# Performance work log

Hardware: AMD Instinct MI355X
Metric: run time of the kernel (lower is better)

Reference implementation:

```python
import jax, jax.numpy as jnp
import numpy as np
from jax import lax

B, T, F = 128, 100, 64
HID = [16, 32]  # encoder hidden dims; decoder uses reversed [32, 16]
K = 3


def _conv2d(x, w, b):
    # x: [N, Cin, H, W], w: [Cout, Cin, kh, kw] -> 'SAME' padding as in torch padding=k//2
    y = lax.conv_general_dilated(x, w, (1, 1), 'SAME',
                                 dimension_numbers=('NCHW', 'OIHW', 'NCHW'))
    return y + b[None, :, None, None]


def _convlstm_layer(xs, w, b, h0, c0):
    # xs: [T, B, Cin, H, W] time-major; returns hidden seq [T,B,Chid,H,W] and final (h, c)
    def step(carry, x_t):
        h, c = carry
        z = _conv2d(jnp.concatenate([x_t, h], axis=1), w, b)
        i, f, o, g = jnp.split(z, 4, axis=1)  # gate order i, f, o, g
        c2 = jax.nn.sigmoid(f) * c + jax.nn.sigmoid(i) * jnp.tanh(g)
        h2 = jax.nn.sigmoid(o) * jnp.tanh(c2)
        return (h2, c2), h2
    (hT, cT), hs = lax.scan(step, (h0, c0), xs)
    return hs, (hT, cT)


def setup_inputs() -> dict:
    key = jax.random.key(0)
    ks = jax.random.split(key, 12)
    s = 0.05
    inp = {
        'x': jax.random.normal(ks[0], (B, T, F), dtype=jnp.float32),
        # encoder layer 0: in=1+16, out=4*16
        'enc_w0': jax.random.normal(ks[1], (4 * HID[0], 1 + HID[0], K, K), dtype=jnp.float32) * s,
        'enc_b0': jnp.zeros((4 * HID[0],), dtype=jnp.float32),
        # encoder layer 1: in=16+32, out=4*32
        'enc_w1': jax.random.normal(ks[2], (4 * HID[1], HID[0] + HID[1], K, K), dtype=jnp.float32) * s,
        'enc_b1': jnp.zeros((4 * HID[1],), dtype=jnp.float32),
        # decoder layer 0: hidden=32, input=32 (last encoder hidden)
        'dec_w0': jax.random.normal(ks[3], (4 * HID[1], HID[1] + HID[1], K, K), dtype=jnp.float32) * s,
        'dec_b0': jnp.zeros((4 * HID[1],), dtype=jnp.float32),
        # decoder layer 1: hidden=16, input=32
        'dec_w1': jax.random.normal(ks[4], (4 * HID[0], HID[1] + HID[0], K, K), dtype=jnp.float32) * s,
        'dec_b1': jnp.zeros((4 * HID[0],), dtype=jnp.float32),
        # final 1x1 conv: 16 -> 1
        'fc_w': jax.random.normal(ks[5], (1, HID[0], 1, 1), dtype=jnp.float32) * s,
        'fc_b': jnp.zeros((1,), dtype=jnp.float32),
    }
    return inp


def reference(x, enc_w0, enc_b0, enc_w1, enc_b1, dec_w0, dec_b0, dec_w1, dec_b1, fc_w, fc_b):
    b, t, f = x.shape
    # [b,t,f] -> [t,b,1,f,1] time-major, spatial (f,1)
    xs = jnp.transpose(x.reshape(b, t, 1, f, 1), (1, 0, 2, 3, 4))
    z16 = jnp.zeros((b, HID[0], f, 1), x.dtype)
    z32 = jnp.zeros((b, HID[1], f, 1), x.dtype)

    enc1, (h1, c1) = _convlstm_layer(xs, enc_w0, enc_b0, z16, z16)
    enc2, (h2, c2) = _convlstm_layer(enc1, enc_w1, enc_b1, z32, z32)

    # decoder initial states = encoder final states reversed
    dec1, _ = _convlstm_layer(enc2, dec_w0, dec_b0, h2, c2)
    dec2, _ = _convlstm_layer(dec1, dec_w1, dec_b1, h1, c1)  # [t,b,16,f,1]

    # final 1x1 conv applied per timestep == one batched conv over t*b
    flat = dec2.reshape(t * b, HID[0], f, 1)
    out = _conv2d(flat, fc_w, fc_b)  # [t*b,1,f,1]
    recon = jnp.transpose(out.reshape(t, b, f), (1, 0, 2))  # [b,t,f]
    return recon
```

## Files before the change

kernel.cpp:

```cpp
#include <hip/hip_runtime.h>
#include <math.h>

#define B_ 128
#define T_ 100
#define RS 72
#define RS2 40

__device__ __forceinline__ float frcp_(float x){ return __builtin_amdgcn_rcpf(x); }
__device__ __forceinline__ float fsig_(float x){ return frcp_(1.f + __expf(-x)); }
__device__ __forceinline__ float ftanh_(float x){ float e = __expf(2.f*x); return 1.f - 2.f*frcp_(e+1.f); }
__device__ __forceinline__ float gate1(float zi, float zf, float zo, float zg, float& c){
    float cc = fsig_(zf)*c + fsig_(zi)*ftanh_(zg);
    c = cc;
    return fsig_(zo)*ftanh_(cc);
}
__device__ __forceinline__ float4 ldf4(const float* p){ return *reinterpret_cast<const float4*>(p); }
__device__ __forceinline__ void stf4(float* p, float4 v){ *reinterpret_cast<float4*>(p) = v; }
__device__ __forceinline__ float2 ldf2(const float* p){ return *reinterpret_cast<const float2*>(p); }
__device__ __forceinline__ void stf2(float* p, float2 v){ *reinterpret_cast<float2*>(p) = v; }
__device__ __forceinline__ float4 add4(float4 a, float4 b){
    return make_float4(a.x+b.x, a.y+b.y, a.z+b.z, a.w+b.w);
}
__device__ __forceinline__ float4 gate4(float4 zi, float4 zf, float4 zo, float4 zg,
                                        float bi, float bf, float bo, float bg, float4& c){
    float4 h;
    h.x = gate1(zi.x+bi, zf.x+bf, zo.x+bo, zg.x+bg, c.x);
    h.y = gate1(zi.y+bi, zf.y+bf, zo.y+bo, zg.y+bg, c.y);
    h.z = gate1(zi.z+bi, zf.z+bf, zo.z+bo, zg.z+bg, c.z);
    h.w = gate1(zi.w+bi, zf.w+bf, zo.w+bo, zg.w+bg, c.w);
    return h;
}

__device__ __forceinline__ void fma4v(float w, float u0,float u1,float u2,float u3, float4& a){
    a.x = fmaf(w,u0,a.x); a.y = fmaf(w,u1,a.y);
    a.z = fmaf(w,u2,a.z); a.w = fmaf(w,u3,a.w);
}
__device__ __forceinline__ void fma2v(float w, float u0,float u1, float2& a){
    a.x = fmaf(w,u0,a.x); a.y = fmaf(w,u1,a.y);
}

template<int ROWS>
__device__ __forceinline__ void rowacc4(const float* __restrict__ rowp,
                                        const float* __restrict__ wk,
                                        float4& ai, float4& af, float4& ao, float4& ag)
{
    float  m = rowp[-1];
    float4 a = ldf4(rowp);
    float  p = rowp[4];
    float4 wa = ldf4(wk);
    float4 wb = ldf4(wk + ROWS);
    float4 wc = ldf4(wk + 2*ROWS);
    fma4v(wa.x, m,a.x,a.y,a.z, ai);  fma4v(wa.y, m,a.x,a.y,a.z, af);
    fma4v(wa.z, m,a.x,a.y,a.z, ao);  fma4v(wa.w, m,a.x,a.y,a.z, ag);
    fma4v(wb.x, a.x,a.y,a.z,a.w, ai); fma4v(wb.y, a.x,a.y,a.z,a.w, af);
    fma4v(wb.z, a.x,a.y,a.z,a.w, ao); fma4v(wb.w, a.x,a.y,a.z,a.w, ag);
    fma4v(wc.x, a.y,a.z,a.w,p, ai);  fma4v(wc.y, a.y,a.z,a.w,p, af);
    fma4v(wc.z, a.y,a.z,a.w,p, ao);  fma4v(wc.w, a.y,a.z,a.w,p, ag);
}
template<int ROWS>
__device__ __forceinline__ void rowacc2(const float* __restrict__ rowp,
                                        const float* __restrict__ wk,
                                        float2& ai, float2& af, float2& ao, float2& ag)
{
    float  m = rowp[-1];
    float2 a = *reinterpret_cast<const float2*>(rowp);
    float  p = rowp[2];
    float4 wa = ldf4(wk);
    float4 wb = ldf4(wk + ROWS);
    float4 wc = ldf4(wk + 2*ROWS);
    fma2v(wa.x, m,a.x, ai); fma2v(wa.y, m,a.x, af);
    fma2v(wa.z, m,a.x, ao); fma2v(wa.w, m,a.x, ag);
    fma2v(wb.x, a.x,a.y, ai); fma2v(wb.y, a.x,a.y, af);
    fma2v(wb.z, a.x,a.y, ao); fma2v(wb.w, a.x,a.y, ag);
    fma2v(wc.x, a.y,p, ai); fma2v(wc.y, a.y,p, af);
    fma2v(wc.z, a.y,p, ao); fma2v(wc.w, a.y,p, ag);
}
template<int ROWS>
__device__ __forceinline__ void rowacc8(const float* __restrict__ rowp,
                                        const float* __restrict__ wk,
                                        float4& i0, float4& i1, float4& f0v, float4& f1v,
                                        float4& o0, float4& o1, float4& g0, float4& g1)
{
    float  m = rowp[-1];
    float4 a = ldf4(rowp);
    float4 b = ldf4(rowp + 4);
    float  p = rowp[8];
    float4 wa = ldf4(wk);
    float4 wb = ldf4(wk + ROWS);
    float4 wc = ldf4(wk + 2*ROWS);
    fma4v(wa.x, m,a.x,a.y,a.z, i0);   fma4v(wa.x, a.w,b.x,b.y,b.z, i1);
    fma4v(wa.y, m,a.x,a.y,a.z, f0v);  fma4v(wa.y, a.w,b.x,b.y,b.z, f1v);
    fma4v(wa.z, m,a.x,a.y,a.z, o0);   fma4v(wa.z, a.w,b.x,b.y,b.z, o1);
    fma4v(wa.w, m,a.x,a.y,a.z, g0);   fma4v(wa.w, a.w,b.x,b.y,b.z, g1);
    fma4v(wb.x, a.x,a.y,a.z,a.w, i0); fma4v(wb.x, b.x,b.y,b.z,b.w, i1);
    fma4v(wb.y, a.x,a.y,a.z,a.w, f0v);fma4v(wb.y, b.x,b.y,b.z,b.w, f1v);
    fma4v(wb.z, a.x,a.y,a.z,a.w, o0); fma4v(wb.z, b.x,b.y,b.z,b.w, o1);
    fma4v(wb.w, a.x,a.y,a.z,a.w, g0); fma4v(wb.w, b.x,b.y,b.z,b.w, g1);
    fma4v(wc.x, a.y,a.z,a.w,b.x, i0); fma4v(wc.x, b.y,b.z,b.w,p, i1);
    fma4v(wc.y, a.y,a.z,a.w,b.x, f0v);fma4v(wc.y, b.y,b.z,b.w,p, f1v);
    fma4v(wc.z, a.y,a.z,a.w,b.x, o0); fma4v(wc.z, b.y,b.z,b.w,p, o1);
    fma4v(wc.w, a.y,a.z,a.w,b.x, g0); fma4v(wc.w, b.y,b.z,b.w,p, g1);
}

__global__ __launch_bounds__(1024, 4) void enc_kernel(
    const float* __restrict__ x,
    const float* __restrict__ w0, const float* __restrict__ b0,
    const float* __restrict__ w1, const float* __restrict__ b1,
    float* __restrict__ seq,
    float* __restrict__ h1f, float* __restrict__ c1f,
    float* __restrict__ h2f, float* __restrict__ c2f,
    float* __restrict__ comm, int* __restrict__ flags)
{
    __shared__ float wl0[51 * 64];
    __shared__ float wl1[144 * 128];
    __shared__ float bs0[64];
    __shared__ float bs1[128];
    __shared__ float hbuf[50 * RS2];
    __shared__ float zsA[2048];
    __shared__ float zsB3[3 * 4096];

    const int tid = threadIdx.x;
    const int b = blockIdx.x & 127;
    const int s = blockIdx.x >> 7;
    const int gofs = s << 5;
    const int g  = tid >> 8;
    const int r  = tid & 255;
    const int chB = r >> 3, f0B = (r & 7) * 4;
    const int chA = r >> 4, f0A = (r & 15) * 2;
    const int haloSlot = s ? 3 : 36;
    const int myId = (b << 1) | s;
    const int peerId = myId ^ 1;
    float* mySend = &comm[(size_t)myId * 128];
    const float* peerBuf = &comm[(size_t)peerId * 128];

    for (int idx = tid; idx < 51 * 64; idx += 1024) {
        int k = idx >> 6, rr = idx & 63;
        int ch = rr >> 2, gg = rr & 3;
        int ci = k / 3, d = k - ci * 3;
        wl0[idx] = w0[((gg * 16 + ch) * 17 + ci) * 9 + d * 3 + 1];
    }
    for (int idx = tid; idx < 144 * 128; idx += 1024) {
        int k = idx >> 7, rr = idx & 127;
        int ch = rr >> 2, gg = rr & 3;
        int ci = k / 3, d = k - ci * 3;
        wl1[idx] = w1[((gg * 32 + ch) * 48 + ci) * 9 + d * 3 + 1];
    }
    if (tid < 64) bs0[tid] = b0[tid];
    if (tid < 128) bs1[tid] = b1[tid];
    for (int i = tid; i < 50 * RS2; i += 1024) hbuf[i] = 0.f;
    __syncthreads();

    const int xl = tid - 256;
    if (xl >= 0 && xl < 34) {
        const int gc = gofs - 1 + xl;
        const bool v = (gc >= 0) && (gc < 64);
        hbuf[0 * RS2 + 3 + xl] = v ? x[(b * T_ + 0) * 64 + gc] : 0.f;
        hbuf[1 * RS2 + 3 + xl] = v ? x[(b * T_ + 1) * 64 + gc] : 0.f;
    }
    const float biA = bs0[chA], bfA = bs0[16+chA], boA = bs0[32+chA], bgA = bs0[48+chA];
    const float biB = bs1[chB], bfB = bs1[32+chB], boB = bs1[64+chB], bgB = bs1[96+chB];
    __syncthreads();

    const float4 z4 = make_float4(0.f, 0.f, 0.f, 0.f);
    const float2 z2 = make_float2(0.f, 0.f);
    float2 c0q = z2;
    float4 c1a = z4;

    if (g == 2) {
        float2 ai = z2, af = z2, ao = z2, ag = z2;
        rowacc2<64>(&hbuf[0 * RS2 + 4 + f0A], &wl0[chA * 4], ai, af, ao, ag);
        float2 hq;
        hq.x = gate1(ai.x + biA, af.x + bfA, ao.x + boA, ag.x + bgA, c0q.x);
        hq.y = gate1(ai.y + biA, af.y + bfA, ao.y + boA, ag.y + bgA, c0q.y);
        *reinterpret_cast<float2*>(&hbuf[(2 + chA) * RS2 + 4 + f0A]) = hq;
        if ((r & 15) == (s ? 0 : 15)) {
            const float v = s ? hq.x : hq.y;
            __hip_atomic_store((unsigned int*)&mySend[1 * 64 + 32 + chA],
                               __float_as_uint(v),
                               __ATOMIC_RELAXED, __HIP_MEMORY_SCOPE_AGENT);
        }
    }
    __syncthreads();

#pragma unroll 1
    for (int t = 0; t < T_; ++t) {
        if (tid == 0)
            __hip_atomic_store(&flags[myId], t + 1,
                               __ATOMIC_RELAXED, __HIP_MEMORY_SCOPE_AGENT);
        if (tid < 48 && (t > 0 || tid >= 32)) {
            while (__hip_atomic_load(&flags[peerId],
                                     __ATOMIC_ACQUIRE, __HIP_MEMORY_SCOPE_AGENT) < t + 1)
                __builtin_amdgcn_s_sleep(2);
            const int par = (t + 1) & 1;
            const unsigned int uv =
                __hip_atomic_load((const unsigned int*)&peerBuf[par * 64 + tid],
                                  __ATOMIC_RELAXED, __HIP_MEMORY_SCOPE_AGENT);
            const float v = __uint_as_float(uv);
            if (tid < 32) hbuf[(18 + tid) * RS2 + haloSlot] = v;
            else          hbuf[(2 + (tid - 32)) * RS2 + haloSlot] = v;
        }
        __syncthreads();

        const bool doL0 = (t + 1 < T_);
        float4 I = z4, F = z4, O = z4, G = z4;
#pragma unroll 1
        for (int j = 0; j < 12; ++j) {
            const int ci = 12 * g + j;
            rowacc4<128>(&hbuf[(2 + ci) * RS2 + 4 + f0B],
                         &wl1[(ci * 3) * 128 + chB * 4], I, F, O, G);
        }
        float2 ai = z2, af = z2, ao = z2, ag = z2;
        if (doL0) {
            if (g == 2) {
                rowacc2<64>(&hbuf[((t + 1) & 1) * RS2 + 4 + f0A], &wl0[chA * 4],
                            ai, af, ao, ag);
#pragma unroll 1
                for (int j = 0; j < 8; ++j)
                    rowacc2<64>(&hbuf[(2 + j) * RS2 + 4 + f0A],
                                &wl0[((1 + j) * 3) * 64 + chA * 4], ai, af, ao, ag);
            } else if (g == 3) {
#pragma unroll 1
                for (int j = 8; j < 16; ++j)
                    rowacc2<64>(&hbuf[(2 + j) * RS2 + 4 + f0A],
                                &wl0[((1 + j) * 3) * 64 + chA * 4], ai, af, ao, ag);
            }
        }
        if (g != 0) {
            float* zp = &zsB3[(g - 1) * 4096 + r * 4];
            stf4(zp, I); stf4(zp + 1024, F); stf4(zp + 2048, O); stf4(zp + 3072, G);
        }
        if (g == 3 && doL0) {
            float* zp = &zsA[r * 2];
            stf2(zp, ai); stf2(zp + 512, af); stf2(zp + 1024, ao); stf2(zp + 1536, ag);
        }
        if (xl >= 0 && xl < 34 && t + 2 < T_) {
            const int gc = gofs - 1 + xl;
            hbuf[(t & 1) * RS2 + 3 + xl] =
                (gc >= 0 && gc < 64) ? x[(b * T_ + t + 2) * 64 + gc] : 0.f;
        }
        __syncthreads();
        if (g == 0) {
            const float* p0 = &zsB3[0 * 4096 + r * 4];
            const float* p1 = &zsB3[1 * 4096 + r * 4];
            const float* p2 = &zsB3[2 * 4096 + r * 4];
            float4 zi = add4(add4(I, ldf4(p0)),        add4(ldf4(p1),        ldf4(p2)));
            float4 zf = add4(add4(F, ldf4(p0 + 1024)), add4(ldf4(p1 + 1024), ldf4(p2 + 1024)));
            float4 zo = add4(add4(O, ldf4(p0 + 2048)), add4(ldf4(p1 + 2048), ldf4(p2 + 2048)));
            float4 zg = add4(add4(G, ldf4(p0 + 3072)), add4(ldf4(p1 + 3072), ldf4(p2 + 3072)));
            float4 hq = gate4(zi, zf, zo, zg, biB, bfB, boB, bgB, c1a);
            stf4(&hbuf[(18 + chB) * RS2 + 4 + f0B], hq);
            stf4(&seq[((size_t)t * B_ + b) * 2048 + chB * 64 + gofs + f0B], hq);
            if (doL0 && (r & 7) == (s ? 0 : 7)) {
                const float v = s ? hq.x : hq.w;
                __hip_atomic_store((unsigned int*)&mySend[(t & 1) * 64 + chB],
                                   __float_as_uint(v),
                                   __ATOMIC_RELAXED, __HIP_MEMORY_SCOPE_AGENT);
            }
        }
        if (g == 2 && doL0) {
            float2 pzi = ldf2(&zsA[r * 2]);
            float2 pzf = ldf2(&zsA[512 + r * 2]);
            float2 pzo = ldf2(&zsA[1024 + r * 2]);
            float2 pzg = ldf2(&zsA[1536 + r * 2]);
            float2 hq2;
            hq2.x = gate1(ai.x+pzi.x+biA, af.x+pzf.x+bfA, ao.x+pzo.x+boA, ag.x+pzg.x+bgA, c0q.x);
            hq2.y = gate1(ai.y+pzi.y+biA, af.y+pzf.y+bfA, ao.y+pzo.y+boA, ag.y+pzg.y+bgA, c0q.y);
            *reinterpret_cast<float2*>(&hbuf[(2 + chA) * RS2 + 4 + f0A]) = hq2;
            if ((r & 15) == (s ? 0 : 15)) {
                const float v = s ? hq2.x : hq2.y;
                __hip_atomic_store((unsigned int*)&mySend[(t & 1) * 64 + 32 + chA],
                                   __float_as_uint(v),
                                   __ATOMIC_RELAXED, __HIP_MEMORY_SCOPE_AGENT);
            }
        }
        __syncthreads();
    }

    if (g == 2) {
        *reinterpret_cast<float2*>(&h1f[(b * 16 + chA) * 64 + gofs + f0A]) =
            *reinterpret_cast<const float2*>(&hbuf[(2 + chA) * RS2 + 4 + f0A]);
        *reinterpret_cast<float2*>(&c1f[(b * 16 + chA) * 64 + gofs + f0A]) = c0q;
    }
    if (g == 0) {
        stf4(&h2f[b * 2048 + chB * 64 + gofs + f0B],
             ldf4(&hbuf[(18 + chB) * RS2 + 4 + f0B]));
        stf4(&c2f[b * 2048 + chB * 64 + gofs + f0B], c1a);
    }
}

__global__ __launch_bounds__(256, 2) void xconv0_kernel(
    const float* __restrict__ seqIn, const float* __restrict__ w,
    float* __restrict__ zx, int t0)
{
    __shared__ float wl[96 * 128];
    __shared__ float xt[32 * RS];

    const int tid = threadIdx.x;
    const int tl = blockIdx.x / B_;
    const int b  = blockIdx.x - tl * B_;
    const int t  = t0 + tl;

    for (int idx = tid; idx < 96 * 128; idx += 256) {
        int k = idx >> 7, rr = idx & 127;
        int ch = rr >> 2, g = rr & 3;
        int ci = k / 3, d = k - ci * 3;
        wl[idx] = w[((g * 32 + ch) * 64 + ci) * 9 + d * 3 + 1];
    }
    {
        int rr = tid >> 3, j = tid & 7;
        xt[rr * RS + (j < 4 ? j : 64 + j)] = 0.f;
    }
    {
        const float* s = &seqIn[((size_t)t * B_ + b) * 2048 + tid * 8];
        float4 v0 = ldf4(s);
        float4 v1 = ldf4(s + 4);
        int ci = tid >> 3, col = (tid & 7) * 8;
        stf4(&xt[ci * RS + 4 + col], v0);
        stf4(&xt[ci * RS + 4 + col + 4], v1);
    }
    __syncthreads();

    const int ch = tid >> 3, f0 = (tid & 7) * 8;
    const float4 z4 = make_float4(0.f,0.f,0.f,0.f);
    float4 i0=z4,i1=z4,f0v=z4,f1v=z4,o0=z4,o1=z4,g0=z4,g1=z4;
#pragma unroll 1
    for (int rr = 0; rr < 32; ++rr)
        rowacc8<128>(&xt[rr * RS + 4 + f0], wl + (rr * 3) * 128 + ch * 4,
                     i0, i1, f0v, f1v, o0, o1, g0, g1);

    float* zp = &zx[(((size_t)tl * B_ + b) * 4) * 2048 + ch * 64 + f0];
    stf4(zp, i0);            stf4(zp + 4, i1);
    stf4(zp + 2048, f0v);    stf4(zp + 2048 + 4, f1v);
    stf4(zp + 4096, o0);     stf4(zp + 4096 + 4, o1);
    stf4(zp + 6144, g0);     stf4(zp + 6144 + 4, g1);
}

__global__ __launch_bounds__(512, 1) void decg(
    const float* __restrict__ w0, const float* __restrict__ b0,
    const float* __restrict__ w1, const float* __restrict__ b1,
    const float* __restrict__ zx,
    const float* __restrict__ h0in, const float* __restrict__ c0in,
    const float* __restrict__ h1in, const float* __restrict__ c1in,
    float* __restrict__ h0sv, float* __restrict__ c0sv,
    float* __restrict__ h1sv, float* __restrict__ c1sv,
    const float* __restrict__ fw, const float* __restrict__ fb,
    float* __restrict__ out,
    float* __restrict__ comm0, float* __restrict__ comm1,
    int* __restrict__ flg, int t0, int tn, int lastc)
{
    __shared__ float wl0[96 * 128];
    __shared__ float wl1[144 * 64];
    __shared__ float hp0[32 * RS2];
    __shared__ float hp1[16 * RS2];
    __shared__ float zs0[4096];
    __shared__ float zs1[4 * 16 * 32];
    __shared__ float bs0[128];
    __shared__ float bs1[64];
    __shared__ float fcw[16];
    __shared__ float fcb_s;

    const int tid = threadIdx.x;
    const int b = blockIdx.x & 127;
    const int s = blockIdx.x >> 7;
    const int gofs = s << 5;
    const int haloSlot = s ? 3 : 36;
    const int bcol = s ? 31 : 32;
    const int myId = (b << 1) | s, peerId = myId ^ 1;
    float* send0 = &comm0[(size_t)myId * 64];
    const float* peer0 = &comm0[(size_t)peerId * 64];
    float* send1 = &comm1[(size_t)myId * 32];
    const float* peer1 = &comm1[(size_t)peerId * 32];

    const int kg = tid >> 8;
    const int r = tid & 255;
    const bool isD0 = (r < 128);
    const int ch0 = r >> 2, t0f = (r & 3) * 8;
    const int r1 = r - 128;
    const int ch1 = r1 >> 3, t1f = (r1 & 7) * 4;

    for (int idx = tid; idx < 96 * 128; idx += 512) {
        int k = idx >> 7, rr = idx & 127;
        int c8 = rr >> 2, g = rr & 3;
        int ci = k / 3, d = k - ci * 3;
        wl0[idx] = w0[((g * 32 + c8) * 64 + 32 + ci) * 9 + d * 3 + 1];
    }
    for (int idx = tid; idx < 144 * 64; idx += 512) {
        int k = idx >> 6, rr = idx & 63;
        int c8 = rr >> 2, g = rr & 3;
        int ci = k / 3, d = k - ci * 3;
        wl1[idx] = w1[((g * 16 + c8) * 48 + ci) * 9 + d * 3 + 1];
    }
    if (tid < 128) bs0[tid] = b0[tid];
    if (tid < 64) bs1[tid] = b1[tid];
    if (tid < 16) fcw[tid] = fw[tid];
    if (tid == 16) fcb_s = fb[0];
    for (int i = tid; i < 32 * RS2; i += 512) hp0[i] = 0.f;
    for (int i = tid; i < 16 * RS2; i += 512) hp1[i] = 0.f;
    __syncthreads();

    for (int i = tid; i < 1024; i += 512) {
        int c8 = i >> 5, f = i & 31;
        hp0[c8 * RS2 + 4 + f] = h0in[b * 2048 + c8 * 64 + gofs + f];
    }
    { int c8 = tid >> 5, f = tid & 31;
      hp1[c8 * RS2 + 4 + f] = h1in[b * 1024 + c8 * 64 + gofs + f]; }
    if (tid < 32) hp0[tid * RS2 + haloSlot] = h0in[b * 2048 + tid * 64 + bcol];
    if (tid >= 64 && tid < 80)
        hp1[(tid - 64) * RS2 + haloSlot] = h1in[b * 1024 + (tid - 64) * 64 + bcol];

    const float4 z4 = make_float4(0.f, 0.f, 0.f, 0.f);
    float4 c0a = z4, c0b = z4;
    float4 c1v = z4;
    float bi, bfv, bo, bg;
    if (isD0) { bi = bs0[ch0]; bfv = bs0[32+ch0]; bo = bs0[64+ch0]; bg = bs0[96+ch0]; }
    else      { bi = bs1[ch1]; bfv = bs1[16+ch1]; bo = bs1[32+ch1]; bg = bs1[48+ch1]; }
    if (kg == 0) {
        if (isD0) {
            c0a = ldf4(&c0in[b * 2048 + ch0 * 64 + gofs + t0f]);
            c0b = ldf4(&c0in[b * 2048 + ch0 * 64 + gofs + t0f + 4]);
        } else {
            c1v = ldf4(&c1in[b * 1024 + ch1 * 64 + gofs + t1f]);
        }
    }
    const float fcbv = fcb_s;

#pragma unroll 1
    for (int u = t0; u < t0 + tn + lastc; ++u) {
        if (tid == 0)
            __hip_atomic_store(&flg[myId], u,
                               __ATOMIC_RELAXED, __HIP_MEMORY_SCOPE_AGENT);
        if (u > t0) {
            const int par = (u - 1) & 1;
            if (tid < 32) {
                while (__hip_atomic_load(&flg[peerId],
                                         __ATOMIC_ACQUIRE, __HIP_MEMORY_SCOPE_AGENT) < u)
                    __builtin_amdgcn_s_sleep(2);
                hp0[tid * RS2 + haloSlot] = __uint_as_float(
                    __hip_atomic_load((const unsigned int*)&peer0[par * 32 + tid],
                                      __ATOMIC_RELAXED, __HIP_MEMORY_SCOPE_AGENT));
            } else if (tid >= 64 && tid < 80 && u >= 2) {
                while (__hip_atomic_load(&flg[peerId],
                                         __ATOMIC_ACQUIRE, __HIP_MEMORY_SCOPE_AGENT) < u)
                    __builtin_amdgcn_s_sleep(2);
                hp1[(tid - 64) * RS2 + haloSlot] = __uint_as_float(
                    __hip_atomic_load((const unsigned int*)&peer1[par * 16 + (tid - 64)],
                                      __ATOMIC_RELAXED, __HIP_MEMORY_SCOPE_AGENT));
            }
        }
        __syncthreads();

        const bool d0act = (u - t0 < tn);
        const bool d1act = (u >= 1);
        float4 A0=z4,A1=z4,B0=z4,B1=z4,C0=z4,C1=z4,D0=z4,D1=z4;
        float4 ai=z4, af=z4, ao=z4, ag=z4;
        float4 X0=z4,X1=z4,X2=z4,X3=z4,X4=z4,X5=z4,X6=z4,X7=z4;

        if (isD0) {
            if (d0act) {
                if (kg == 0) {
                    const float* zp = &zx[(((size_t)(u - t0) * B_ + b) * 4) * 2048
                                          + ch0 * 64 + gofs + t0f];
                    X0 = ldf4(zp);         X1 = ldf4(zp + 4);
                    X2 = ldf4(zp + 2048);  X3 = ldf4(zp + 2052);
                    X4 = ldf4(zp + 4096);  X5 = ldf4(zp + 4100);
                    X6 = ldf4(zp + 6144);  X7 = ldf4(zp + 6148);
                }
#pragma unroll 1
                for (int j = 0; j < 16; ++j) {
                    const int ci = kg * 16 + j;
                    rowacc8<128>(&hp0[ci * RS2 + 4 + t0f], &wl0[(ci * 3) * 128 + ch0 * 4],
                                 A0, A1, B0, B1, C0, C1, D0, D1);
                }
            }
            if (kg == 1 && r < 32 && u >= 2) {
                float a = fcbv;
#pragma unroll
                for (int k2 = 0; k2 < 16; ++k2)
                    a = fmaf(fcw[k2], hp1[k2 * RS2 + 4 + r], a);
                out[(b * T_ + (u - 2)) * 64 + gofs + r] = a;
            }
        } else if (d1act) {
            if (kg == 0) {
#pragma unroll 1
                for (int j = 0; j < 24; ++j)
                    rowacc4<64>(&hp0[j * RS2 + 4 + t1f], &wl1[(j * 3) * 64 + ch1 * 4],
                                ai, af, ao, ag);
            } else {
#pragma unroll 1
                for (int j = 24; j < 32; ++j)
                    rowacc4<64>(&hp0[j * RS2 + 4 + t1f], &wl1[(j * 3) * 64 + ch1 * 4],
                                ai, af, ao, ag);
#pragma unroll 1
                for (int j = 0; j < 16; ++j)
                    rowacc4<64>(&hp1[j * RS2 + 4 + t1f], &wl1[((32 + j) * 3) * 64 + ch1 * 4],
                                ai, af, ao, ag);
            }
        }
        if (kg == 1) {
            if (isD0) { if (d0act) {
                float* zp = &zs0[r * 4];
                stf4(zp + 0,    A0); stf4(zp + 512,  A1);
                stf4(zp + 1024, B0); stf4(zp + 1536, B1);
                stf4(zp + 2048, C0); stf4(zp + 2560, C1);
                stf4(zp + 3072, D0); stf4(zp + 3584, D1);
            }} else { if (d1act) {
                stf4(&zs1[(0*16+ch1)*32 + t1f], ai);
                stf4(&zs1[(1*16+ch1)*32 + t1f], af);
                stf4(&zs1[(2*16+ch1)*32 + t1f], ao);
                stf4(&zs1[(3*16+ch1)*32 + t1f], ag);
            }}
        }
        __syncthreads();
        if (kg == 0) {
            if (isD0 && d0act) {
                const float* zp = &zs0[r * 4];
                float4 zi0 = add4(add4(A0, X0), ldf4(zp));
                float4 zi1 = add4(add4(A1, X1), ldf4(zp + 512));
                float4 zf0 = add4(add4(B0, X2), ldf4(zp + 1024));
                float4 zf1 = add4(add4(B1, X3), ldf4(zp + 1536));
                float4 zo0 = add4(add4(C0, X4), ldf4(zp + 2048));
                float4 zo1 = add4(add4(C1, X5), ldf4(zp + 2560));
                float4 zg0 = add4(add4(D0, X6), ldf4(zp + 3072));
                float4 zg1 = add4(add4(D1, X7), ldf4(zp + 3584));
                float4 h0q0 = gate4(zi0, zf0, zo0, zg0, bi, bfv, bo, bg, c0a);
                float4 h0q1 = gate4(zi1, zf1, zo1, zg1, bi, bfv, bo, bg, c0b);
                stf4(&hp0[ch0 * RS2 + 4 + t0f], h0q0);
                stf4(&hp0[ch0 * RS2 + 4 + t0f + 4], h0q1);
                if ((r & 3) == (s ? 0 : 3)) {
                    __hip_atomic_store((unsigned int*)&send0[(u & 1) * 32 + ch0],
                                       __float_as_uint(s ? h0q0.x : h0q1.w),
                                       __ATOMIC_RELAXED, __HIP_MEMORY_SCOPE_AGENT);
                }
            } else if (!isD0 && d1act) {
                float4 zi = add4(ai, ldf4(&zs1[(0*16+ch1)*32 + t1f]));
                float4 zf = add4(af, ldf4(&zs1[(1*16+ch1)*32 + t1f]));
                float4 zo = add4(ao, ldf4(&zs1[(2*16+ch1)*32 + t1f]));
                float4 zg = add4(ag, ldf4(&zs1[(3*16+ch1)*32 + t1f]));
                float4 h1q = gate4(zi, zf, zo, zg, bi, bfv, bo, bg, c1v);
                stf4(&hp1[ch1 * RS2 + 4 + t1f], h1q);
                if ((r1 & 7) == (s ? 0 : 7)) {
                    __hip_atomic_store((unsigned int*)&send1[(u & 1) * 16 + ch1],
                                       __float_as_uint(s ? h1q.x : h1q.w),
                                       __ATOMIC_RELAXED, __HIP_MEMORY_SCOPE_AGENT);
                }
            }
        }
        __syncthreads();
    }

    if (lastc && tid < 32) {
        float a = fcbv;
#pragma unroll
        for (int k2 = 0; k2 < 16; ++k2)
            a = fmaf(fcw[k2], hp1[k2 * RS2 + 4 + tid], a);
        out[(b * T_ + (T_ - 1)) * 64 + gofs + tid] = a;
    }
    for (int i = tid; i < 1024; i += 512) {
        int c8 = i >> 5, f = i & 31;
        h0sv[b * 2048 + c8 * 64 + gofs + f] = hp0[c8 * RS2 + 4 + f];
    }
    { int c8 = tid >> 5, f = tid & 31;
      h1sv[b * 1024 + c8 * 64 + gofs + f] = hp1[c8 * RS2 + 4 + f]; }
    if (kg == 0) {
        if (isD0) {
            stf4(&c0sv[b * 2048 + ch0 * 64 + gofs + t0f], c0a);
            stf4(&c0sv[b * 2048 + ch0 * 64 + gofs + t0f + 4], c0b);
        } else {
            stf4(&c1sv[b * 1024 + ch1 * 64 + gofs + t1f], c1v);
        }
    }
}

__global__ __launch_bounds__(512, 1) void dec0_fb(
    const float* __restrict__ w, const float* __restrict__ bias,
    float* __restrict__ seq,
    const float* __restrict__ hin, const float* __restrict__ cin)
{
    __shared__ float wl[192 * 128];
    __shared__ float bs[128];
    __shared__ float xin[32 * RS];
    __shared__ float hp[32 * RS];

    const int tid = threadIdx.x;
    const int b = blockIdx.x;

    for (int idx = tid; idx < 192 * 128; idx += 512) {
        int k = idx >> 7, rr = idx & 127;
        int ch = rr >> 2, g = rr & 3;
        int ci = k / 3, d = k - ci * 3;
        wl[idx] = w[((g * 32 + ch) * 64 + ci) * 9 + d * 3 + 1];
    }
    if (tid < 128) bs[tid] = bias[tid];
    for (int i = tid; i < 32 * RS; i += 512) { xin[i] = 0.f; hp[i] = 0.f; }
    __syncthreads();
    {
        const float* hs = &hin[b * 2048 + tid * 4];
        float4 hv = ldf4(hs);
        int ci = tid >> 4, col = (tid & 15) * 4;
        stf4(&hp[ci * RS + 4 + col], hv);
    }
    const int ch = tid >> 4, f0 = (tid & 15) * 4;
    float4 cc = ldf4(&cin[b * 2048 + ch * 64 + f0]);
    const float bi = bs[ch], bf = bs[32 + ch], bo = bs[64 + ch], bg = bs[96 + ch];
    const float4 z4 = make_float4(0.f,0.f,0.f,0.f);

    float4 nx = ldf4(&seq[(size_t)b * 2048 + tid * 4]);

#pragma unroll 1
    for (int t = 0; t < T_; ++t) {
        {
            int ci = tid >> 4, col = (tid & 15) * 4;
            stf4(&xin[ci * RS + 4 + col], nx);
        }
        __syncthreads();
        if (t + 1 < T_)
            nx = ldf4(&seq[((size_t)(t + 1) * B_ + b) * 2048 + tid * 4]);
        float4 ai = z4, af = z4, ao = z4, ag = z4;
#pragma unroll 1
        for (int rr = 0; rr < 32; ++rr)
            rowacc4<128>(&xin[rr * RS + 4 + f0], wl + (rr * 3) * 128 + ch * 4, ai, af, ao, ag);
#pragma unroll 1
        for (int rr = 0; rr < 32; ++rr)
            rowacc4<128>(&hp[rr * RS + 4 + f0], wl + ((32 + rr) * 3) * 128 + ch * 4, ai, af, ao, ag);
        float4 hn = gate4(ai, af, ao, ag, bi, bf, bo, bg, cc);
        __syncthreads();
        stf4(&hp[ch * RS + 4 + f0], hn);
        stf4(&seq[((size_t)t * B_ + b) * 2048 + ch * 64 + f0], hn);
    }
}

__global__ __launch_bounds__(512, 1) void dec1_fb(
    const float* __restrict__ w, const float* __restrict__ bias,
    const float* __restrict__ seq,
    const float* __restrict__ hin, const float* __restrict__ cin,
    const float* __restrict__ fw, const float* __restrict__ fb,
    float* __restrict__ out)
{
    __shared__ float wl[144 * 64];
    __shared__ float bs[64];
    __shared__ float xin[32 * RS];
    __shared__ float hp[16 * RS];
    __shared__ float fcw[16];
    __shared__ float fcb;

    const int tid = threadIdx.x;
    const int b = blockIdx.x;

    for (int idx = tid; idx < 144 * 64; idx += 512) {
        int k = idx >> 6, rr = idx & 63;
        int ch = rr >> 2, g = rr & 3;
        int ci = k / 3, d = k - ci * 3;
        wl[idx] = w[((g * 16 + ch) * 48 + ci) * 9 + d * 3 + 1];
    }
    if (tid < 64) bs[tid] = bias[tid];
    if (tid < 16) fcw[tid] = fw[tid];
    if (tid == 16) fcb = fb[0];
    for (int i = tid; i < 32 * RS; i += 512) xin[i] = 0.f;
    for (int i = tid; i < 16 * RS; i += 512) hp[i] = 0.f;
    __syncthreads();
    {
        const float* hs = &hin[b * 1024 + tid * 2];
        float2 hv = *reinterpret_cast<const float2*>(hs);
        int ci = tid >> 5, col = (tid & 31) * 2;
        *reinterpret_cast<float2*>(&hp[ci * RS + 4 + col]) = hv;
    }
    const int ch = tid >> 5, f0 = (tid & 31) * 2;
    float2 cc = *reinterpret_cast<const float2*>(&cin[b * 1024 + ch * 64 + f0]);
    const float bi = bs[ch], bf = bs[16 + ch], bo = bs[32 + ch], bg = bs[48 + ch];
    const float2 z2 = make_float2(0.f,0.f);
    float4 nx = ldf4(&seq[(size_t)b * 2048 + tid * 4]);
    __syncthreads();

#pragma unroll 1
    for (int t = 0; t < T_; ++t) {
        {
            int ci = tid >> 4, col = (tid & 15) * 4;
            stf4(&xin[ci * RS + 4 + col], nx);
        }
        __syncthreads();
        if (t + 1 < T_)
            nx = ldf4(&seq[((size_t)(t + 1) * B_ + b) * 2048 + tid * 4]);

        float2 ai = z2, af = z2, ao = z2, ag = z2;
#pragma unroll 1
        for (int rr = 0; rr < 32; ++rr)
            rowacc2<64>(&xin[rr * RS + 4 + f0], wl + (rr * 3) * 64 + ch * 4, ai, af, ao, ag);
#pragma unroll 1
        for (int rr = 0; rr < 16; ++rr)
            rowacc2<64>(&hp[rr * RS + 4 + f0], wl + ((32 + rr) * 3) * 64 + ch * 4, ai, af, ao, ag);

        float2 hh;
        hh.x = gate1(ai.x + bi, af.x + bf, ao.x + bo, ag.x + bg, cc.x);
        hh.y = gate1(ai.y + bi, af.y + bf, ao.y + bo, ag.y + bg, cc.y);
        __syncthreads();
        *reinterpret_cast<float2*>(&hp[ch * RS + 4 + f0]) = hh;
        __syncthreads();

        if (tid < 64) {
            float a = fcb;
#pragma unroll
            for (int k2 = 0; k2 < 16; ++k2)
                a = fmaf(fcw[k2], hp[k2 * RS + 4 + tid], a);
            out[(b * T_ + t) * 64 + tid] = a;
        }
    }
}

extern "C" void kernel_launch(void* const* d_in, const int* in_sizes, int n_in,
                              void* d_out, int out_size, void* d_ws, size_t ws_size,
                              hipStream_t stream)
{
    (void)in_sizes; (void)n_in; (void)out_size;
    const float* x   = (const float*)d_in[0];
    const float* ew0 = (const float*)d_in[1];
    const float* eb0 = (const float*)d_in[2];
    const float* ew1 = (const float*)d_in[3];
    const float* eb1 = (const float*)d_in[4];
    const float* dw0 = (const float*)d_in[5];
    const float* db0 = (const float*)d_in[6];
    const float* dw1 = (const float*)d_in[7];
    const float* db1 = (const float*)d_in[8];
    const float* fw  = (const float*)d_in[9];
    const float* fb  = (const float*)d_in[10];
    float* out = (float*)d_out;

    float* ws  = (float*)d_ws;
    size_t off = 0;
    float* seq = ws + off; off += (size_t)T_ * B_ * 2048;
    float* h1f = ws + off; off += (size_t)B_ * 1024;
    float* c1f = ws + off; off += (size_t)B_ * 1024;
    float* h2f = ws + off; off += (size_t)B_ * 2048;
    float* c2f = ws + off; off += (size_t)B_ * 2048;
    float* hd0 = ws + off; off += (size_t)B_ * 2048;
    float* cd0 = ws + off; off += (size_t)B_ * 2048;
    float* hd1 = ws + off; off += (size_t)B_ * 1024;
    float* cd1 = ws + off; off += (size_t)B_ * 1024;
    float* comm = ws + off; off += 32768 + 16384 + 8192;
    int*   flg  = (int*)(ws + off); off += 1024;
    float* zx  = ws + off;

    float* commD0 = comm + 32768;
    float* commD1 = comm + 32768 + 16384;

    size_t availf = (ws_size / 4 > off) ? (ws_size / 4 - off) : 0;
    int TC = 0;
    if      (availf >= (size_t)100 * B_ * 8192) TC = 100;
    else if (availf >= (size_t)50  * B_ * 8192) TC = 50;
    else if (availf >= (size_t)25  * B_ * 8192) TC = 25;
    else if (availf >= (size_t)10  * B_ * 8192) TC = 10;

    hipMemsetAsync(flg, 0, 512 * sizeof(int), stream);
    enc_kernel<<<256, 1024, 0, stream>>>(x, ew0, eb0, ew1, eb1, seq,
                                         h1f, c1f, h2f, c2f, comm, flg);

    if (TC > 0) {
        for (int t0 = 0; t0 < T_; t0 += TC) {
            int tn = (t0 + TC <= T_) ? TC : (T_ - t0);
            int lastc = (t0 + tn >= T_) ? 1 : 0;
            xconv0_kernel<<<tn * B_, 256, 0, stream>>>(seq, dw0, zx, t0);
            decg<<<256, 512, 0, stream>>>(
                dw0, db0, dw1, db1, zx,
                t0 == 0 ? h2f : hd0, t0 == 0 ? c2f : cd0,
                t0 == 0 ? h1f : hd1, t0 == 0 ? c1f : cd1,
                hd0, cd0, hd1, cd1,
                fw, fb, out, commD0, commD1, flg + 256, t0, tn, lastc);
        }
    } else {
        dec0_fb<<<B_, 512, 0, stream>>>(dw0, db0, seq, h2f, c2f);
        dec1_fb<<<B_, 512, 0, stream>>>(dw1, db1, seq, h1f, c1f, fw, fb, out);
    }
}
```

Measured before the change: 2.008 ms.

## Double decoder block threads and split recurrent conv reductions across more groups

The fused decoder kernel now runs with 1024 threads per block instead of 512. Decoder layer 0 gives each thread 4 output columns instead of 8. Decoder layer 1 splits its 48 input rows across four 12-row groups and sums the partials through a larger shared-memory buffer. The goal is to shorten the per-timestep critical path of this latency-bound serial recurrence by spreading each step over more threads. In exchange it adds more partial-sum shared-memory traffic. The launch bound of (1024, 4) may also force a tight register budget and cause spills.

New measurement: 1.940 ms. -3.4%, faster.

```diff
diff --git a/kernel.cpp b/kernel.cpp
--- a/kernel.cpp
+++ b/kernel.cpp
@@ -335,7 +335,7 @@
     stf4(zp + 6144, g0);     stf4(zp + 6144 + 4, g1);
 }
 
-__global__ __launch_bounds__(512, 1) void decg(
+__global__ __launch_bounds__(1024, 4) void decg(
     const float* __restrict__ w0, const float* __restrict__ b0,
     const float* __restrict__ w1, const float* __restrict__ b1,
     const float* __restrict__ zx,
@@ -353,7 +353,7 @@
     __shared__ float hp0[32 * RS2];
     __shared__ float hp1[16 * RS2];
     __shared__ float zs0[4096];
-    __shared__ float zs1[4 * 16 * 32];
+    __shared__ float zs1_3[3 * 2048];
     __shared__ float bs0[128];
     __shared__ float bs1[64];
     __shared__ float fcw[16];
@@ -371,20 +371,22 @@
     float* send1 = &comm1[(size_t)myId * 32];
     const float* peer1 = &comm1[(size_t)peerId * 32];
 
-    const int kg = tid >> 8;
-    const int r = tid & 255;
-    const bool isD0 = (r < 128);
-    const int ch0 = r >> 2, t0f = (r & 3) * 8;
-    const int r1 = r - 128;
-    const int ch1 = r1 >> 3, t1f = (r1 & 7) * 4;
-
-    for (int idx = tid; idx < 96 * 128; idx += 512) {
+    const bool isD0 = (tid < 512);
+    const int sub = tid & 511;
+    const int kg = sub >> 8;
+    const int r = sub & 255;
+    const int ch0 = r >> 3, t0f = (r & 7) * 4;
+    const int d1g = sub >> 7;
+    const int rg1 = sub & 127;
+    const int ch1 = rg1 >> 3, t1f = (rg1 & 7) * 4;
+
+    for (int idx = tid; idx < 96 * 128; idx += 1024) {
         int k = idx >> 7, rr = idx & 127;
         int c8 = rr >> 2, g = rr & 3;
         int ci = k / 3, d = k - ci * 3;
         wl0[idx] = w0[((g * 32 + c8) * 64 + 32 + ci) * 9 + d * 3 + 1];
     }
-    for (int idx = tid; idx < 144 * 64; idx += 512) {
+    for (int idx = tid; idx < 144 * 64; idx += 1024) {
         int k = idx >> 6, rr = idx & 63;
         int c8 = rr >> 2, g = rr & 3;
         int ci = k / 3, d = k - ci * 3;
@@ -394,34 +396,31 @@
     if (tid < 64) bs1[tid] = b1[tid];
     if (tid < 16) fcw[tid] = fw[tid];
     if (tid == 16) fcb_s = fb[0];
-    for (int i = tid; i < 32 * RS2; i += 512) hp0[i] = 0.f;
-    for (int i = tid; i < 16 * RS2; i += 512) hp1[i] = 0.f;
+    for (int i = tid; i < 32 * RS2; i += 1024) hp0[i] = 0.f;
+    for (int i = tid; i < 16 * RS2; i += 1024) hp1[i] = 0.f;
     __syncthreads();
 
-    for (int i = tid; i < 1024; i += 512) {
-        int c8 = i >> 5, f = i & 31;
+    {
+        int c8 = tid >> 5, f = tid & 31;
         hp0[c8 * RS2 + 4 + f] = h0in[b * 2048 + c8 * 64 + gofs + f];
-    }
-    { int c8 = tid >> 5, f = tid & 31;
-      hp1[c8 * RS2 + 4 + f] = h1in[b * 1024 + c8 * 64 + gofs + f]; }
+        if (tid < 512)
+            hp1[(tid >> 5) * RS2 + 4 + (tid & 31)] =
+                h1in[b * 1024 + (tid >> 5) * 64 + gofs + (tid & 31)];
+    }
     if (tid < 32) hp0[tid * RS2 + haloSlot] = h0in[b * 2048 + tid * 64 + bcol];
     if (tid >= 64 && tid < 80)
         hp1[(tid - 64) * RS2 + haloSlot] = h1in[b * 1024 + (tid - 64) * 64 + bcol];
 
     const float4 z4 = make_float4(0.f, 0.f, 0.f, 0.f);
-    float4 c0a = z4, c0b = z4;
+    float4 c0v = z4;
     float4 c1v = z4;
     float bi, bfv, bo, bg;
     if (isD0) { bi = bs0[ch0]; bfv = bs0[32+ch0]; bo = bs0[64+ch0]; bg = bs0[96+ch0]; }
     else      { bi = bs1[ch1]; bfv = bs1[16+ch1]; bo = bs1[32+ch1]; bg = bs1[48+ch1]; }
-    if (kg == 0) {
-        if (isD0) {
-            c0a = ldf4(&c0in[b * 2048 + ch0 * 64 + gofs + t0f]);
-            c0b = ldf4(&c0in[b * 2048 + ch0 * 64 + gofs + t0f + 4]);
-        } else {
-            c1v = ldf4(&c1in[b * 1024 + ch1 * 64 + gofs + t1f]);
-        }
-    }
+    if (isD0 && kg == 0)
+        c0v = ldf4(&c0in[b * 2048 + ch0 * 64 + gofs + t0f]);
+    if (!isD0 && d1g == 0)
+        c1v = ldf4(&c1in[b * 1024 + ch1 * 64 + gofs + t1f]);
     const float fcbv = fcb_s;
 
 #pragma unroll 1
@@ -451,25 +450,24 @@
 
         const bool d0act = (u - t0 < tn);
         const bool d1act = (u >= 1);
-        float4 A0=z4,A1=z4,B0=z4,B1=z4,C0=z4,C1=z4,D0=z4,D1=z4;
-        float4 ai=z4, af=z4, ao=z4, ag=z4;
-        float4 X0=z4,X1=z4,X2=z4,X3=z4,X4=z4,X5=z4,X6=z4,X7=z4;
+        float4 ai = z4, af = z4, ao = z4, ag = z4;
+        float4 xi = z4, xf = z4, xo = z4, xg = z4;
 
         if (isD0) {
             if (d0act) {
                 if (kg == 0) {
                     const float* zp = &zx[(((size_t)(u - t0) * B_ + b) * 4) * 2048
                                           + ch0 * 64 + gofs + t0f];
-                    X0 = ldf4(zp);         X1 = ldf4(zp + 4);
-                    X2 = ldf4(zp + 2048);  X3 = ldf4(zp + 2052);
-                    X4 = ldf4(zp + 4096);  X5 = ldf4(zp + 4100);
-                    X6 = ldf4(zp + 6144);  X7 = ldf4(zp + 6148);
+                    xi = ldf4(zp);
+                    xf = ldf4(zp + 2048);
+                    xo = ldf4(zp + 4096);
+                    xg = ldf4(zp + 6144);
                 }
 #pragma unroll 1
                 for (int j = 0; j < 16; ++j) {
                     const int ci = kg * 16 + j;
-                    rowacc8<128>(&hp0[ci * RS2 + 4 + t0f], &wl0[(ci * 3) * 128 + ch0 * 4],
-                                 A0, A1, B0, B1, C0, C1, D0, D1);
+                    rowacc4<128>(&hp0[ci * RS2 + 4 + t0f], &wl0[(ci * 3) * 128 + ch0 * 4],
+                                 ai, af, ao, ag);
                 }
             }
             if (kg == 1 && r < 32 && u >= 2) {
@@ -480,69 +478,57 @@
                 out[(b * T_ + (u - 2)) * 64 + gofs + r] = a;
             }
         } else if (d1act) {
-            if (kg == 0) {
-#pragma unroll 1
-                for (int j = 0; j < 24; ++j)
-                    rowacc4<64>(&hp0[j * RS2 + 4 + t1f], &wl1[(j * 3) * 64 + ch1 * 4],
-                                ai, af, ao, ag);
-            } else {
-#pragma unroll 1
-                for (int j = 24; j < 32; ++j)
-                    rowacc4<64>(&hp0[j * RS2 + 4 + t1f], &wl1[(j * 3) * 64 + ch1 * 4],
-                                ai, af, ao, ag);
-#pragma unroll 1
-                for (int j = 0; j < 16; ++j)
-                    rowacc4<64>(&hp1[j * RS2 + 4 + t1f], &wl1[((32 + j) * 3) * 64 + ch1 * 4],
-                                ai, af, ao, ag);
-            }
-        }
-        if (kg == 1) {
-            if (isD0) { if (d0act) {
+            const int rlo = 12 * d1g, rhi = rlo + 12;
+            const int xhi = rhi < 32 ? rhi : 32;
+            const int hlo = rlo > 32 ? rlo : 32;
+#pragma unroll 1
+            for (int rr = rlo; rr < xhi; ++rr)
+                rowacc4<64>(&hp0[rr * RS2 + 4 + t1f], &wl1[(rr * 3) * 64 + ch1 * 4],
+                            ai, af, ao, ag);
+#pragma unroll 1
+            for (int rr = hlo; rr < rhi; ++rr)
+                rowacc4<64>(&hp1[(rr - 32) * RS2 + 4 + t1f], &wl1[(rr * 3) * 64 + ch1 * 4],
+                            ai, af, ao, ag);
+        }
+        if (isD0) {
+            if (kg == 1 && d0act) {
                 float* zp = &zs0[r * 4];
-                stf4(zp + 0,    A0); stf4(zp + 512,  A1);
-                stf4(zp + 1024, B0); stf4(zp + 1536, B1);
-                stf4(zp + 2048, C0); stf4(zp + 2560, C1);
-                stf4(zp + 3072, D0); stf4(zp + 3584, D1);
-            }} else { if (d1act) {
-                stf4(&zs1[(0*16+ch1)*32 + t1f], ai);
-                stf4(&zs1[(1*16+ch1)*32 + t1f], af);
-                stf4(&zs1[(2*16+ch1)*32 + t1f], ao);
-                stf4(&zs1[(3*16+ch1)*32 + t1f], ag);
-            }}
-        }
-        __syncthreads();
-        if (kg == 0) {
-            if (isD0 && d0act) {
-                const float* zp = &zs0[r * 4];
-                float4 zi0 = add4(add4(A0, X0), ldf4(zp));
-                float4 zi1 = add4(add4(A1, X1), ldf4(zp + 512));
-                float4 zf0 = add4(add4(B0, X2), ldf4(zp + 1024));
-                float4 zf1 = add4(add4(B1, X3), ldf4(zp + 1536));
-                float4 zo0 = add4(add4(C0, X4), ldf4(zp + 2048));
-                float4 zo1 = add4(add4(C1, X5), ldf4(zp + 2560));
-                float4 zg0 = add4(add4(D0, X6), ldf4(zp + 3072));
-                float4 zg1 = add4(add4(D1, X7), ldf4(zp + 3584));
-                float4 h0q0 = gate4(zi0, zf0, zo0, zg0, bi, bfv, bo, bg, c0a);
-                float4 h0q1 = gate4(zi1, zf1, zo1, zg1, bi, bfv, bo, bg, c0b);
-                stf4(&hp0[ch0 * RS2 + 4 + t0f], h0q0);
-                stf4(&hp0[ch0 * RS2 + 4 + t0f + 4], h0q1);
-                if ((r & 3) == (s ? 0 : 3)) {
-                    __hip_atomic_store((unsigned int*)&send0[(u & 1) * 32 + ch0],
-                                       __float_as_uint(s ? h0q0.x : h0q1.w),
-                                       __ATOMIC_RELAXED, __HIP_MEMORY_SCOPE_AGENT);
-                }
-            } else if (!isD0 && d1act) {
-                float4 zi = add4(ai, ldf4(&zs1[(0*16+ch1)*32 + t1f]));
-                float4 zf = add4(af, ldf4(&zs1[(1*16+ch1)*32 + t1f]));
-                float4 zo = add4(ao, ldf4(&zs1[(2*16+ch1)*32 + t1f]));
-                float4 zg = add4(ag, ldf4(&zs1[(3*16+ch1)*32 + t1f]));
-                float4 h1q = gate4(zi, zf, zo, zg, bi, bfv, bo, bg, c1v);
-                stf4(&hp1[ch1 * RS2 + 4 + t1f], h1q);
-                if ((r1 & 7) == (s ? 0 : 7)) {
-                    __hip_atomic_store((unsigned int*)&send1[(u & 1) * 16 + ch1],
-                                       __float_as_uint(s ? h1q.x : h1q.w),
-                                       __ATOMIC_RELAXED, __HIP_MEMORY_SCOPE_AGENT);
-                }
+                stf4(zp, ai); stf4(zp + 1024, af);
+                stf4(zp + 2048, ao); stf4(zp + 3072, ag);
+            }
+        } else if (d1g != 0 && d1act) {
+            float* zp = &zs1_3[(d1g - 1) * 2048 + rg1 * 4];
+            stf4(zp, ai); stf4(zp + 512, af);
+            stf4(zp + 1024, ao); stf4(zp + 1536, ag);
+        }
+        __syncthreads();
+        if (isD0 && kg == 0 && d0act) {
+            const float* zp = &zs0[r * 4];
+            float4 zi4 = add4(add4(ai, xi), ldf4(zp));
+            float4 zf4 = add4(add4(af, xf), ldf4(zp + 1024));
+            float4 zo4 = add4(add4(ao, xo), ldf4(zp + 2048));
+            float4 zg4 = add4(add4(ag, xg), ldf4(zp + 3072));
+            float4 h0q = gate4(zi4, zf4, zo4, zg4, bi, bfv, bo, bg, c0v);
+            stf4(&hp0[ch0 * RS2 + 4 + t0f], h0q);
+            if ((r & 7) == (s ? 0 : 7)) {
+                __hip_atomic_store((unsigned int*)&send0[(u & 1) * 32 + ch0],
+                                   __float_as_uint(s ? h0q.x : h0q.w),
+                                   __ATOMIC_RELAXED, __HIP_MEMORY_SCOPE_AGENT);
+            }
+        } else if (!isD0 && d1g == 0 && d1act) {
+            const float* p0 = &zs1_3[0 * 2048 + rg1 * 4];
+            const float* p1 = &zs1_3[1 * 2048 + rg1 * 4];
+            const float* p2 = &zs1_3[2 * 2048 + rg1 * 4];
+            float4 zi4 = add4(add4(ai, ldf4(p0)),        add4(ldf4(p1),        ldf4(p2)));
+            float4 zf4 = add4(add4(af, ldf4(p0 + 512)),  add4(ldf4(p1 + 512),  ldf4(p2 + 512)));
+            float4 zo4 = add4(add4(ao, ldf4(p0 + 1024)), add4(ldf4(p1 + 1024), ldf4(p2 + 1024)));
+            float4 zg4 = add4(add4(ag, ldf4(p0 + 1536)), add4(ldf4(p1 + 1536), ldf4(p2 + 1536)));
+            float4 h1q = gate4(zi4, zf4, zo4, zg4, bi, bfv, bo, bg, c1v);
+            stf4(&hp1[ch1 * RS2 + 4 + t1f], h1q);
+            if ((rg1 & 7) == (s ? 0 : 7)) {
+                __hip_atomic_store((unsigned int*)&send1[(u & 1) * 16 + ch1],
+                                   __float_as_uint(s ? h1q.x : h1q.w),
+                                   __ATOMIC_RELAXED, __HIP_MEMORY_SCOPE_AGENT);
             }
         }
         __syncthreads();
@@ -555,20 +541,17 @@
             a = fmaf(fcw[k2], hp1[k2 * RS2 + 4 + tid], a);
         out[(b * T_ + (T_ - 1)) * 64 + gofs + tid] = a;
     }
-    for (int i = tid; i < 1024; i += 512) {
-        int c8 = i >> 5, f = i & 31;
+    {
+        int c8 = tid >> 5, f = tid & 31;
         h0sv[b * 2048 + c8 * 64 + gofs + f] = hp0[c8 * RS2 + 4 + f];
-    }
-    { int c8 = tid >> 5, f = tid & 31;
-      h1sv[b * 1024 + c8 * 64 + gofs + f] = hp1[c8 * RS2 + 4 + f]; }
-    if (kg == 0) {
-        if (isD0) {
-            stf4(&c0sv[b * 2048 + ch0 * 64 + gofs + t0f], c0a);
-            stf4(&c0sv[b * 2048 + ch0 * 64 + gofs + t0f + 4], c0b);
-        } else {
-            stf4(&c1sv[b * 1024 + ch1 * 64 + gofs + t1f], c1v);
-        }
-    }
+        if (tid < 512)
+            h1sv[b * 1024 + (tid >> 5) * 64 + gofs + (tid & 31)] =
+                hp1[(tid >> 5) * RS2 + 4 + (tid & 31)];
+    }
+    if (isD0 && kg == 0)
+        stf4(&c0sv[b * 2048 + ch0 * 64 + gofs + t0f], c0v);
+    if (!isD0 && d1g == 0)
+        stf4(&c1sv[b * 1024 + ch1 * 64 + gofs + t1f], c1v);
 }
 
 __global__ __launch_bounds__(512, 1) void dec0_fb(
@@ -758,7 +741,7 @@
             int tn = (t0 + TC <= T_) ? TC : (T_ - t0);
             int lastc = (t0 + tn >= T_) ? 1 : 0;
             xconv0_kernel<<<tn * B_, 256, 0, stream>>>(seq, dw0, zx, t0);
-            decg<<<256, 512, 0, stream>>>(
+            decg<<<256, 1024, 0, stream>>>(
                 dw0, db0, dw1, db1, zx,
                 t0 == 0 ? h2f : hd0, t0 == 0 ? c2f : cd0,
                 t0 == 0 ? h1f : hd1, t0 == 0 ? c1f : cd1,
```
